# Kernel tuning notes

Hardware: AMD Instinct MI355X
Metric: run time of the kernel (lower is better)

The kernel has to match this reference:

```python
import jax, jax.numpy as jnp
import numpy as np

# Model dims (hardcoded by the hw-accurate numerics: >>6 mean -> d_model=64, 45/256 ~ 1/sqrt(32) -> head_dim=32)
D_MODEL = 64; N_HEADS = 2; HEAD_DIM = 32; D_FF = 256
N_LAYERS = 4; VOCAB = 8192; CTX = 1024; B = 4; T = 1024


def _ste(x, y):
    # forward value y, straight-through gradient of x
    return x + jax.lax.stop_gradient(y - x)


def ste_round_clamp(x, lo, hi):
    return _ste(x, jnp.clip(jnp.round(x), lo, hi))


def ste_round_clamp_int8(x):
    return ste_round_clamp(x, -128.0, 127.0)


def ste_shift_right(x, n):
    s = x * (0.5 ** n)
    return _ste(s, jnp.floor(s))


def ste_hw_int8(x):
    # hardware truncation to signed 8 bits (wrap-around, not clamp)
    return _ste(x, jnp.mod(x + 128.0, 256.0) - 128.0)


def bitlinear_hw(x, w):
    # ternary weights via STE (BitNet b1.58 style), int accumulate, >>6 requant, int8 clamp
    scale = jnp.maximum(jnp.mean(jnp.abs(w)), 1e-5)
    w_t = ste_round_clamp(w / scale, -1.0, 1.0)
    acc = jnp.einsum('btc,oc->bto', x, w_t)
    return ste_round_clamp_int8(ste_shift_right(acc, 6))


def rmsnorm_hw(x, weight):
    x_int = ste_round_clamp_int8(x)
    sum_sq = jnp.sum(x_int * x_int, axis=-1, keepdims=True)
    mean_sq = ste_shift_right(sum_sq, 6)                       # /64 == /d_model
    lut_idx = jnp.clip(ste_shift_right(mean_sq, 6), 0.0, 255.0)
    bin_center = jnp.maximum(lut_idx * 64.0 + 32.0, 1.0)
    inv_rms = ste_round_clamp(16384.0 / jnp.sqrt(bin_center), 0.0, 16383.0)
    w_c = weight + jax.lax.stop_gradient(jnp.clip(weight, -2.0, 2.0) - weight)
    gamma_q = ste_round_clamp(w_c * 1024.0, -32768.0, 32767.0)  # Q5.10
    p1 = ste_shift_right(x_int * inv_rms, 8)
    y = ste_shift_right(p1 * gamma_q, 10)
    return ste_round_clamp_int8(y)


def hw_softmax(scores):
    # 4-segment piecewise-linear exp + uint8 normalization (Softmax.scala)
    m = jnp.max(scores, axis=-1, keepdims=True)
    sh = scores - m
    ea = jnp.where(sh >= -3.0, 256.0 + sh * 64.0,
         jnp.where(sh >= -8.0, 64.0 + (sh + 3.0) * 11.0,
         jnp.where(sh >= -24.0, sh + 24.0, 0.0)))
    s = jnp.maximum(jnp.sum(ea, axis=-1, keepdims=True), 1.0)
    return ste_round_clamp(ea / s * 255.0, 0.0, 255.0)


def _forward(tokens, tok_emb, pos_emb, attn_norm_w, q_w, k_w, v_w, o_w,
             ff_norm_w, up_w, down_w, final_norm_w):
    positions = jnp.arange(T)
    tok_q = ste_round_clamp(tok_emb[tokens] * 1024.0, -32768.0, 32767.0)
    pos_q = ste_round_clamp(pos_emb[positions] * 1024.0, -32768.0, 32767.0)
    x = ste_hw_int8(ste_shift_right(tok_q + pos_q[None], 3))   # [B,T,D]
    causal = jnp.triu(jnp.ones((T, T), dtype=bool), k=1)
    for i in range(N_LAYERS):
        # attention block
        h = rmsnorm_hw(x, attn_norm_w[i])
        q = bitlinear_hw(h, q_w[i]).reshape(B, T, N_HEADS, HEAD_DIM).transpose(0, 2, 1, 3)
        k = bitlinear_hw(h, k_w[i]).reshape(B, T, N_HEADS, HEAD_DIM).transpose(0, 2, 1, 3)
        v = bitlinear_hw(h, v_w[i]).reshape(B, T, N_HEADS, HEAD_DIM).transpose(0, 2, 1, 3)
        scores = ste_shift_right(jnp.einsum('bhqd,bhkd->bhqk', q, k) * 45.0, 8)
        scores = jnp.where(causal, -32767.0, scores)
        probs = hw_softmax(scores)                              # uint8-valued
        a = ste_hw_int8(ste_shift_right(jnp.einsum('bhqk,bhkd->bhqd', probs, v), 8))
        a = a.transpose(0, 2, 1, 3).reshape(B, T, D_MODEL)
        a = bitlinear_hw(a, o_w[i])
        x = ste_hw_int8(x + a)
        # FFN block
        h = rmsnorm_hw(x, ff_norm_w[i])
        u = ste_round_clamp_int8(jax.nn.relu(bitlinear_hw(h, up_w[i])))
        x = ste_hw_int8(x + bitlinear_hw(u, down_w[i]))
    x = rmsnorm_hw(x, final_norm_w)
    # hw logits: INT8 activations x Q5.10 tied embedding, dequant + 1/sqrt(d) scale
    emb_q = ste_round_clamp(tok_emb * 1024.0, -32768.0, 32767.0)
    logits = jnp.einsum('btd,vd->btv', x, emb_q) * (D_MODEL ** -0.5 / 1024.0)
    return logits


def setup_inputs() -> dict:
    key = jax.random.key(0)
    ks = jax.random.split(key, 12)
    std = 0.02
    inp = {
        'tokens': jax.random.randint(ks[0], (B, T), 0, VOCAB),
        'tok_emb': jax.random.normal(ks[1], (VOCAB, D_MODEL), jnp.float32),  # default N(0,1)
        'pos_emb': std * jax.random.normal(ks[2], (CTX, D_MODEL), jnp.float32),
        'attn_norm_w': jnp.ones((N_LAYERS, D_MODEL), jnp.float32),
        'q_w': std * jax.random.normal(ks[3], (N_LAYERS, D_MODEL, D_MODEL), jnp.float32),
        'k_w': std * jax.random.normal(ks[4], (N_LAYERS, D_MODEL, D_MODEL), jnp.float32),
        'v_w': std * jax.random.normal(ks[5], (N_LAYERS, D_MODEL, D_MODEL), jnp.float32),
        'o_w': std * jax.random.normal(ks[6], (N_LAYERS, D_MODEL, D_MODEL), jnp.float32),
        'ff_norm_w': jnp.ones((N_LAYERS, D_MODEL), jnp.float32),
        'up_w': std * jax.random.normal(ks[7], (N_LAYERS, D_FF, D_MODEL), jnp.float32),
        'down_w': std * jax.random.normal(ks[8], (N_LAYERS, D_MODEL, D_FF), jnp.float32),
        'final_norm_w': jnp.ones((D_MODEL,), jnp.float32),
    }
    return inp


def reference(tokens, tok_emb, pos_emb, attn_norm_w, q_w, k_w, v_w, o_w,
              ff_norm_w, up_w, down_w, final_norm_w):
    return _forward(tokens, tok_emb, pos_emb, attn_norm_w, q_w, k_w, v_w, o_w,
                    ff_norm_w, up_w, down_w, final_norm_w)
```

## Files before the change

### kernel.cpp

```cpp
#include <hip/hip_runtime.h>
#include <stdint.h>

#define T_CTX 1024
#define DM 64
#define NH 2
#define HD 32
#define DFF 256
#define NVOCAB 8192

typedef int v4i __attribute__((ext_vector_type(4)));

__device__ __forceinline__ int clampi(int v, int lo, int hi){ return v<lo?lo:(v>hi?hi:v); }
__device__ __forceinline__ int wrap8(int v){ return ((v + 128) & 255) - 128; }
__device__ __forceinline__ int sdot4(int a, int b, int c){ return __builtin_amdgcn_sdot4(a, b, c, false); }

__device__ __forceinline__ int wave_reduce_add(int v){
  #pragma unroll
  for (int off = 1; off < 64; off <<= 1) v += __shfl_xor(v, off, 64);
  return v;
}
__device__ __forceinline__ int wave_reduce_max(int v){
  #pragma unroll
  for (int off = 1; off < 64; off <<= 1){ int o = __shfl_xor(v, off, 64); v = o > v ? o : v; }
  return v;
}

__device__ __forceinline__ int rmsnorm_one(int xv, int g){
  int ss  = wave_reduce_add(xv * xv);
  int ms  = ss >> 6;
  int lut = ms >> 6; if (lut > 255) lut = 255;
  int bc  = lut * 64 + 32;
  int inv = (int)__builtin_rint(16384.0 / __builtin_sqrt((double)bc));
  int p1  = (xv * inv) >> 8;
  int y   = (p1 * g) >> 10;
  return clampi(y, -128, 127);
}

__global__ __launch_bounds__(256) void prep_weights(
    const float* __restrict__ qw, const float* __restrict__ kw, const float* __restrict__ vw,
    const float* __restrict__ ow, const float* __restrict__ uw, const float* __restrict__ dw,
    const float* __restrict__ anw, const float* __restrict__ fnw, const float* __restrict__ finw,
    int8_t* __restrict__ wt, int16_t* __restrict__ gq)
{
  int tid = threadIdx.x;
  int bid = blockIdx.x;
  if (bid < 24) {
    int layer = bid / 6, kind = bid % 6;
    const float* src; int n; int off;
    switch (kind) {
      case 0:  src = qw + layer*4096;  n = 4096;  off = 0;     break;
      case 1:  src = kw + layer*4096;  n = 4096;  off = 4096;  break;
      case 2:  src = vw + layer*4096;  n = 4096;  off = 8192;  break;
      case 3:  src = ow + layer*4096;  n = 4096;  off = 12288; break;
      case 4:  src = uw + layer*16384; n = 16384; off = 16384; break;
      default: src = dw + layer*16384; n = 16384; off = 32768; break;
    }
    __shared__ double sred[256];
    double s = 0.0;
    for (int i = tid; i < n; i += 256) s += (double)__builtin_fabsf(src[i]);
    sred[tid] = s; __syncthreads();
    for (int st = 128; st > 0; st >>= 1){ if (tid < st) sred[tid] += sred[tid + st]; __syncthreads(); }
    float fs = (float)(sred[0] / (double)n);
    if (fs < 1e-5f) fs = 1e-5f;
    int8_t* dst = wt + layer*49152 + off;
    for (int i = tid; i < n; i += 256) {
      int t = (int)__builtin_rintf(src[i] / fs);
      dst[i] = (int8_t)clampi(t, -1, 1);
    }
  } else {
    for (int i = tid; i < 576; i += 256) {
      int norm = i >> 6, c = i & 63;
      const float* wsrc = (norm < 4) ? (anw + norm*64) : (norm < 8) ? (fnw + (norm-4)*64) : finw;
      float wv = wsrc[c];
      float wc = wv < -2.0f ? -2.0f : (wv > 2.0f ? 2.0f : wv);
      gq[i] = (int16_t)clampi((int)__builtin_rintf(wc * 1024.0f), -32768, 32767);
    }
  }
}

__global__ __launch_bounds__(256) void prep_emb_kernel(
    const float* __restrict__ tok_emb, int8_t* __restrict__ elo, int8_t* __restrict__ ehi)
{
  int i = blockIdx.x * 256 + threadIdx.x;
  if (i < NVOCAB * DM) {
    int e  = clampi((int)__builtin_rintf(tok_emb[i] * 1024.0f), -32768, 32767);
    int l  = ((e + 128) & 255) - 128;
    int hh = (e - l) >> 8;
    if (hh > 127) hh = 127;
    elo[i] = (int8_t)l; ehi[i] = (int8_t)hh;
  }
}

__global__ __launch_bounds__(256) void token_stage(
    const int* __restrict__ tokens, const float* __restrict__ tok_emb, const float* __restrict__ pos_emb,
    int8_t* __restrict__ x, const int8_t* __restrict__ aArr,
    int8_t* __restrict__ qA, int8_t* __restrict__ kA, int8_t* __restrict__ vT,
    const int8_t* __restrict__ wt, const int16_t* __restrict__ gq, int8_t* __restrict__ xf,
    int do_embed, int post_layer, int pre_layer, int do_final)
{
  __shared__ int8_t sh8[4][DFF];
  int w = threadIdx.x >> 6, lane = threadIdx.x & 63;
  int t = blockIdx.x * 4 + w;
  int8_t* myS = sh8[w];
  int xv;
  if (do_embed) {
    int tok = tokens[t];
    int s = t & (T_CTX - 1);
    int tq = clampi((int)__builtin_rintf(tok_emb[tok*DM + lane] * 1024.0f), -32768, 32767);
    int pq = clampi((int)__builtin_rintf(pos_emb[s*DM + lane] * 1024.0f), -32768, 32767);
    xv = wrap8((tq + pq) >> 3);
  } else {
    xv = (int)x[t*DM + lane];
  }
  if (post_layer >= 0) {
    const int8_t* wtL = wt + post_layer*49152;
    myS[lane] = aArr[t*DM + lane];
    __syncthreads();
    {
      const int* a4 = (const int*)myS;
      const int* wo = (const int*)(wtL + 12288);
      int acc = 0;
      #pragma unroll
      for (int i = 0; i < 16; i++) acc = sdot4(a4[i], wo[lane*16 + i], acc);
      xv = wrap8(xv + clampi(acc >> 6, -128, 127));
    }
    __syncthreads();
    int h2 = rmsnorm_one(xv, (int)gq[(4 + post_layer)*DM + lane]);
    myS[lane] = (int8_t)h2;
    __syncthreads();
    int uv[4];
    {
      const int* h4 = (const int*)myS;
      const int* wu = (const int*)(wtL + 16384);
      #pragma unroll
      for (int jj = 0; jj < 4; jj++) {
        int j = jj*64 + lane;
        int acc = 0;
        #pragma unroll
        for (int i = 0; i < 16; i++) acc = sdot4(h4[i], wu[j*16 + i], acc);
        int u = clampi(acc >> 6, -128, 127);
        uv[jj] = u < 0 ? 0 : u;
      }
    }
    __syncthreads();
    #pragma unroll
    for (int jj = 0; jj < 4; jj++) myS[jj*64 + lane] = (int8_t)uv[jj];
    __syncthreads();
    {
      const int* u4 = (const int*)myS;
      const int* wd = (const int*)(wtL + 32768);
      int acc = 0;
      #pragma unroll
      for (int i = 0; i < 64; i++) acc = sdot4(u4[i], wd[lane*64 + i], acc);
      xv = wrap8(xv + clampi(acc >> 6, -128, 127));
    }
    __syncthreads();
  }
  x[t*DM + lane] = (int8_t)xv;
  if (pre_layer >= 0) {
    int h = rmsnorm_one(xv, (int)gq[pre_layer*DM + lane]);
    myS[lane] = (int8_t)h;
    __syncthreads();
    const int8_t* wtL = wt + pre_layer*49152;
    const int* h4 = (const int*)myS;
    int b = t >> 10, s = t & (T_CTX - 1);
    int hh = lane >> 5, d = lane & 31;
    int bhh = b*NH + hh;
    {
      const int* wm = (const int*)(wtL + 0);
      int acc = 0;
      #pragma unroll
      for (int i = 0; i < 16; i++) acc = sdot4(h4[i], wm[lane*16 + i], acc);
      qA[(bhh*T_CTX + s)*HD + d] = (int8_t)clampi(acc >> 6, -128, 127);
    }
    {
      const int* wm = (const int*)(wtL + 4096);
      int acc = 0;
      #pragma unroll
      for (int i = 0; i < 16; i++) acc = sdot4(h4[i], wm[lane*16 + i], acc);
      kA[(bhh*T_CTX + s)*HD + d] = (int8_t)clampi(acc >> 6, -128, 127);
    }
    {
      const int* wm = (const int*)(wtL + 8192);
      int acc = 0;
      #pragma unroll
      for (int i = 0; i < 16; i++) acc = sdot4(h4[i], wm[lane*16 + i], acc);
      vT[(bhh*HD + d)*T_CTX + s] = (int8_t)clampi(acc >> 6, -128, 127);
    }
  }
  if (do_final) {
    int h = rmsnorm_one(xv, (int)gq[8*DM + lane]);
    xf[t*DM + lane] = (int8_t)h;
  }
}

__global__ __launch_bounds__(256) void attn_kernel(
    const int8_t* __restrict__ qA, const int8_t* __restrict__ kA, const int8_t* __restrict__ vT,
    int8_t* __restrict__ aOut)
{
  __shared__ int vt32[32*257];
  __shared__ int sp32[4][256];
  int w = threadIdx.x >> 6, lane = threadIdx.x & 63;
  int bh = blockIdx.x & 7, qblk = blockIdx.x >> 3;
  int qi = 1023 - 4*qblk - w;
  int b = bh >> 1, h = bh & 1;
  const int8_t* qBase = qA + bh*(T_CTX*HD);
  const int8_t* kBase = kA + bh*(T_CTX*HD);
  const int8_t* vTbh  = vT + bh*(HD*T_CTX);

  #pragma unroll
  for (int r = 0; r < 8; r++) {
    int d = r*4 + w;
    int4 v = *(const int4*)(vTbh + d*T_CTX + lane*16);
    int* dst = vt32 + d*257 + lane*4;
    dst[0] = v.x; dst[1] = v.y; dst[2] = v.z; dst[3] = v.w;
  }

  const int4* qr = (const int4*)(qBase + qi*HD);
  int4 qa = qr[0], qb = qr[1];
  int sc[16];
  int mloc = -(1 << 30);
  #pragma unroll
  for (int j = 0; j < 16; j++) {
    int k = lane + j*64;
    int s;
    if (k <= qi) {
      const int4* kr = (const int4*)(kBase + k*HD);
      int4 ka = kr[0], kb = kr[1];
      int d = 0;
      d = sdot4(qa.x, ka.x, d); d = sdot4(qa.y, ka.y, d);
      d = sdot4(qa.z, ka.z, d); d = sdot4(qa.w, ka.w, d);
      d = sdot4(qb.x, kb.x, d); d = sdot4(qb.y, kb.y, d);
      d = sdot4(qb.z, kb.z, d); d = sdot4(qb.w, kb.w, d);
      s = (d * 45) >> 8;
    } else s = -(1 << 30);
    sc[j] = s; if (s > mloc) mloc = s;
  }
  int m = wave_reduce_max(mloc);
  int ssum = 0;
  #pragma unroll
  for (int j = 0; j < 16; j++) {
    int k = lane + j*64;
    int e = 0;
    if (k <= qi) {
      int sh = sc[j] - m;
      e = (sh >= -3) ? (256 + sh*64)
        : (sh >= -8) ? (64 + (sh + 3)*11)
        : (sh >= -24) ? (sh + 24) : 0;
    }
    sc[j] = e; ssum += e;
  }
  int s0 = wave_reduce_add(ssum); if (s0 < 1) s0 = 1;
  float sf = (float)s0;
  uint8_t* spb = (uint8_t*)sp32[w];
  #pragma unroll
  for (int j = 0; j < 16; j++) {
    int k = lane + j*64;
    int p = (int)__builtin_rintf((float)sc[j] / sf * 255.0f);
    spb[k] = (uint8_t)clampi(p, 0, 255);
  }
  __syncthreads();

  int dg = lane & 7, kc = lane >> 3;
  const int* vr0 = vt32 + (dg*4 + 0)*257;
  const int* vr1 = vt32 + (dg*4 + 1)*257;
  const int* vr2 = vt32 + (dg*4 + 2)*257;
  const int* vr3 = vt32 + (dg*4 + 3)*257;
  const int* spw = sp32[w];
  int hi0=0, hi1=0, hi2=0, hi3=0, lo0=0, lo1=0, lo2=0, lo3=0;
  int cmax = qi >> 2;
  for (int c = kc; c <= cmax; c += 8) {
    int p4 = spw[c];
    int ph = (p4 >> 1) & 0x7f7f7f7f;
    int pl = p4 & 0x01010101;
    int v0 = vr0[c], v1 = vr1[c], v2 = vr2[c], v3 = vr3[c];
    hi0 = sdot4(ph, v0, hi0); lo0 = sdot4(pl, v0, lo0);
    hi1 = sdot4(ph, v1, hi1); lo1 = sdot4(pl, v1, lo1);
    hi2 = sdot4(ph, v2, hi2); lo2 = sdot4(pl, v2, lo2);
    hi3 = sdot4(ph, v3, hi3); lo3 = sdot4(pl, v3, lo3);
  }
  int a0 = 2*hi0 + lo0, a1 = 2*hi1 + lo1, a2 = 2*hi2 + lo2, a3 = 2*hi3 + lo3;
  #pragma unroll
  for (int off = 8; off < 64; off <<= 1) {
    a0 += __shfl_xor(a0, off, 64);
    a1 += __shfl_xor(a1, off, 64);
    a2 += __shfl_xor(a2, off, 64);
    a3 += __shfl_xor(a3, off, 64);
  }
  if (kc == 0) {
    int r0 = wrap8(a0 >> 8) & 255;
    int r1 = wrap8(a1 >> 8) & 255;
    int r2 = wrap8(a2 >> 8) & 255;
    int r3 = wrap8(a3 >> 8) & 255;
    int packed = r0 | (r1 << 8) | (r2 << 16) | (r3 << 24);
    *(int*)(aOut + (b*T_CTX + qi)*DM + h*HD + dg*4) = packed;
  }
}

__global__ __launch_bounds__(256) void logits_kernel(
    const int8_t* __restrict__ xf, const int8_t* __restrict__ elo, const int8_t* __restrict__ ehi,
    float* __restrict__ out)
{
  int w = threadIdx.x >> 6, lane = threadIdx.x & 63;
  int m = lane & 15, quad = lane >> 4;
  int tokBase = blockIdx.y * 64 + w * 16;
  v4i A = *(const v4i*)(xf + (tokBase + m)*DM + quad*16);
  #pragma unroll
  for (int tile = 0; tile < 8; tile++) {
    int vocBase = blockIdx.x * 128 + tile * 16;
    v4i Blo = *(const v4i*)(elo + (vocBase + m)*DM + quad*16);
    v4i Bhi = *(const v4i*)(ehi + (vocBase + m)*DM + quad*16);
    v4i zero = {0, 0, 0, 0};
    v4i dLo = __builtin_amdgcn_mfma_i32_16x16x64_i8(A, Blo, zero, 0, 0, 0);
    v4i dHi = __builtin_amdgcn_mfma_i32_16x16x64_i8(A, Bhi, zero, 0, 0, 0);
    #pragma unroll
    for (int r = 0; r < 4; r++) {
      int val = dLo[r] + (dHi[r] << 8);
      int row = tokBase + quad*4 + r;
      int col = vocBase + m;
      out[row*NVOCAB + col] = (float)val * 1.220703125e-4f;
    }
  }
}

extern "C" void kernel_launch(void* const* d_in, const int* in_sizes, int n_in,
                              void* d_out, int out_size, void* d_ws, size_t ws_size,
                              hipStream_t stream)
{
  const int*   tokens  = (const int*)d_in[0];
  const float* tok_emb = (const float*)d_in[1];
  const float* pos_emb = (const float*)d_in[2];
  const float* attn_nw = (const float*)d_in[3];
  const float* q_w     = (const float*)d_in[4];
  const float* k_w     = (const float*)d_in[5];
  const float* v_w     = (const float*)d_in[6];
  const float* o_w     = (const float*)d_in[7];
  const float* ff_nw   = (const float*)d_in[8];
  const float* up_w    = (const float*)d_in[9];
  const float* dn_w    = (const float*)d_in[10];
  const float* fin_nw  = (const float*)d_in[11];
  float* out = (float*)d_out;
  char* ws = (char*)d_ws;

  int8_t*  x   = (int8_t*)(ws + 0);
  int8_t*  a   = (int8_t*)(ws + 262144);
  int8_t*  qA  = (int8_t*)(ws + 524288);
  int8_t*  kA  = (int8_t*)(ws + 786432);
  int8_t*  vT  = (int8_t*)(ws + 1048576);
  int8_t*  wt  = (int8_t*)(ws + 1310720);
  int8_t*  elo = (int8_t*)(ws + 1507328);
  int8_t*  ehi = (int8_t*)(ws + 2031616);
  int16_t* gq  = (int16_t*)(ws + 2555904);
  int8_t*  xf  = (int8_t*)(ws + 2560000);

  prep_weights<<<25, 256, 0, stream>>>(q_w, k_w, v_w, o_w, up_w, dn_w, attn_nw, ff_nw, fin_nw, wt, gq);
  prep_emb_kernel<<<2048, 256, 0, stream>>>(tok_emb, elo, ehi);
  token_stage<<<1024, 256, 0, stream>>>(tokens, tok_emb, pos_emb, x, a, qA, kA, vT, wt, gq, xf,
                                        1, -1, 0, 0);
  for (int L = 0; L < 4; L++) {
    attn_kernel<<<2048, 256, 0, stream>>>(qA, kA, vT, a);
    int pre = (L < 3) ? (L + 1) : -1;
    int fin = (L == 3) ? 1 : 0;
    token_stage<<<1024, 256, 0, stream>>>(tokens, tok_emb, pos_emb, x, a, qA, kA, vT, wt, gq, xf,
                                          0, L, pre, fin);
  }
  logits_kernel<<<dim3(64, 64), 256, 0, stream>>>(xf, elo, ehi, out);
}
```

Baseline: 358.7 us.

## Fuse prep, embed, attention and token stages into one persistent kernel with grid barriers

Replaces eleven separate launches (weight prep, embedding prep, token stages, attention) with one persistent 512-block kernel that steps through the phases, separated by an atomic grid-wide barrier. Each block now handles 16 queries in attention, so the V tile staged in shared memory is reused across them, and each wave processes two tokens in the per-token stage. The aim is to remove launch gaps and cut redundant V loads. The cost is spin-wait barriers that assume all 512 blocks are co-resident, less parallelism per phase, and serialized query loops inside each block.

```diff
diff --git a/kernel.cpp b/kernel.cpp
--- a/kernel.cpp
+++ b/kernel.cpp
@@ -7,6 +7,7 @@
 #define HD 32
 #define DFF 256
 #define NVOCAB 8192
+#define NBLOCKS 512
 
 typedef int v4i __attribute__((ext_vector_type(4)));
 
@@ -23,6 +24,23 @@
   #pragma unroll
   for (int off = 1; off < 64; off <<= 1){ int o = __shfl_xor(v, off, 64); v = o > v ? o : v; }
   return v;
+}
+
+__device__ __forceinline__ void gbar(int* cnt, int* gen){
+  __syncthreads();
+  if (threadIdx.x == 0) {
+    int g = __hip_atomic_load(gen, __ATOMIC_RELAXED, __HIP_MEMORY_SCOPE_AGENT);
+    int prev = __hip_atomic_fetch_add(cnt, 1, __ATOMIC_ACQ_REL, __HIP_MEMORY_SCOPE_AGENT);
+    if (prev == NBLOCKS - 1) {
+      __hip_atomic_store(cnt, 0, __ATOMIC_RELAXED, __HIP_MEMORY_SCOPE_AGENT);
+      __hip_atomic_store(gen, g + 1, __ATOMIC_RELEASE, __HIP_MEMORY_SCOPE_AGENT);
+    } else {
+      while (__hip_atomic_load(gen, __ATOMIC_ACQUIRE, __HIP_MEMORY_SCOPE_AGENT) == g) {
+        __builtin_amdgcn_s_sleep(8);
+      }
+    }
+  }
+  __syncthreads();
 }
 
 __device__ __forceinline__ int rmsnorm_one(int xv, int g){
@@ -36,14 +54,213 @@
   return clampi(y, -128, 127);
 }
 
-__global__ __launch_bounds__(256) void prep_weights(
-    const float* __restrict__ qw, const float* __restrict__ kw, const float* __restrict__ vw,
-    const float* __restrict__ ow, const float* __restrict__ uw, const float* __restrict__ dw,
-    const float* __restrict__ anw, const float* __restrict__ fnw, const float* __restrict__ finw,
-    int8_t* __restrict__ wt, int16_t* __restrict__ gq)
-{
-  int tid = threadIdx.x;
-  int bid = blockIdx.x;
+__device__ __forceinline__ void do_qkv(int t, int xv, int L, int lane, int8_t* myS,
+    const int8_t* wt, const int16_t* gq, int8_t* qA, int8_t* kA, int8_t* vT)
+{
+  int h = rmsnorm_one(xv, (int)gq[L*DM + lane]);
+  myS[lane] = (int8_t)h;
+  __syncthreads();
+  const int8_t* wtL = wt + L*49152;
+  const int* h4 = (const int*)myS;
+  const int* wq = (const int*)(wtL + 0);
+  const int* wk = (const int*)(wtL + 4096);
+  const int* wv = (const int*)(wtL + 8192);
+  int b = t >> 10, s = t & (T_CTX - 1);
+  int hh = lane >> 5, d = lane & 31;
+  int bhh = b*NH + hh;
+  int accq = 0, acck = 0, accv = 0;
+  #pragma unroll
+  for (int i = 0; i < 16; i++) {
+    int hv = h4[i];
+    accq = sdot4(hv, wq[lane*16 + i], accq);
+    acck = sdot4(hv, wk[lane*16 + i], acck);
+    accv = sdot4(hv, wv[lane*16 + i], accv);
+  }
+  qA[(bhh*T_CTX + s)*HD + d] = (int8_t)clampi(accq >> 6, -128, 127);
+  kA[(bhh*T_CTX + s)*HD + d] = (int8_t)clampi(acck >> 6, -128, 127);
+  vT[(bhh*HD + d)*T_CTX + s] = (int8_t)clampi(accv >> 6, -128, 127);
+}
+
+__device__ __forceinline__ void attn_phase(int bid, int w, int lane,
+    const int8_t* __restrict__ qA, const int8_t* __restrict__ kA,
+    const int8_t* __restrict__ vT, int8_t* __restrict__ aOut, char* smemc)
+{
+  int bh = bid & 7, qgrp = bid >> 3;
+  int b = bh >> 1, h = bh & 1;
+  const int8_t* qBase = qA + bh*(T_CTX*HD);
+  const int8_t* kBase = kA + bh*(T_CTX*HD);
+  const int8_t* vTbh  = vT + bh*(HD*T_CTX);
+  int* vt32 = (int*)smemc;
+  #pragma unroll
+  for (int r = 0; r < 8; r++) {
+    int d = r*4 + w;
+    int4 v = *(const int4*)(vTbh + d*T_CTX + lane*16);
+    int* dst = vt32 + d*257 + lane*4;
+    dst[0] = v.x; dst[1] = v.y; dst[2] = v.z; dst[3] = v.w;
+  }
+  __syncthreads();
+  uint8_t* spb = (uint8_t*)(smemc + 32896 + w*1024);
+  const int* spw = (const int*)spb;
+  int dg = lane & 7, kc = lane >> 3;
+  const int* vr0 = vt32 + (dg*4 + 0)*257;
+  const int* vr1 = vt32 + (dg*4 + 1)*257;
+  const int* vr2 = vt32 + (dg*4 + 2)*257;
+  const int* vr3 = vt32 + (dg*4 + 3)*257;
+  #pragma unroll
+  for (int ri = 0; ri < 4; ri++) {
+    int i = w + ri*4;
+    int qi = i*64 + qgrp;
+    const int4* qr = (const int4*)(qBase + qi*HD);
+    int4 qa = qr[0], qb = qr[1];
+    int sc[16];
+    int mloc = -(1 << 30);
+    #pragma unroll
+    for (int j = 0; j < 16; j++) {
+      int k = lane + j*64;
+      int s;
+      if (k <= qi) {
+        const int4* kr = (const int4*)(kBase + k*HD);
+        int4 ka = kr[0], kb = kr[1];
+        int d0 = 0, d1 = 0;
+        d0 = sdot4(qa.x, ka.x, d0); d1 = sdot4(qa.y, ka.y, d1);
+        d0 = sdot4(qa.z, ka.z, d0); d1 = sdot4(qa.w, ka.w, d1);
+        d0 = sdot4(qb.x, kb.x, d0); d1 = sdot4(qb.y, kb.y, d1);
+        d0 = sdot4(qb.z, kb.z, d0); d1 = sdot4(qb.w, kb.w, d1);
+        s = ((d0 + d1) * 45) >> 8;
+      } else s = -(1 << 30);
+      sc[j] = s; if (s > mloc) mloc = s;
+    }
+    int m = wave_reduce_max(mloc);
+    int ssum = 0;
+    #pragma unroll
+    for (int j = 0; j < 16; j++) {
+      int k = lane + j*64;
+      int e = 0;
+      if (k <= qi) {
+        int sh = sc[j] - m;
+        e = (sh >= -3) ? (256 + sh*64)
+          : (sh >= -8) ? (64 + (sh + 3)*11)
+          : (sh >= -24) ? (sh + 24) : 0;
+      }
+      sc[j] = e; ssum += e;
+    }
+    int s0 = wave_reduce_add(ssum); if (s0 < 1) s0 = 1;
+    float sf = (float)s0;
+    #pragma unroll
+    for (int j = 0; j < 16; j++) {
+      int k = lane + j*64;
+      int p = (int)__builtin_rintf((float)sc[j] / sf * 255.0f);
+      spb[k] = (uint8_t)clampi(p, 0, 255);
+    }
+    __syncthreads();
+    int hi0=0, hi1=0, hi2=0, hi3=0, lo0=0, lo1=0, lo2=0, lo3=0;
+    int cmax = qi >> 2;
+    for (int c = kc; c <= cmax; c += 8) {
+      int p4 = spw[c];
+      int ph = (p4 >> 1) & 0x7f7f7f7f;
+      int pl = p4 & 0x01010101;
+      int v0 = vr0[c], v1 = vr1[c], v2 = vr2[c], v3 = vr3[c];
+      hi0 = sdot4(ph, v0, hi0); lo0 = sdot4(pl, v0, lo0);
+      hi1 = sdot4(ph, v1, hi1); lo1 = sdot4(pl, v1, lo1);
+      hi2 = sdot4(ph, v2, hi2); lo2 = sdot4(pl, v2, lo2);
+      hi3 = sdot4(ph, v3, hi3); lo3 = sdot4(pl, v3, lo3);
+    }
+    int a0 = 2*hi0 + lo0, a1 = 2*hi1 + lo1, a2 = 2*hi2 + lo2, a3 = 2*hi3 + lo3;
+    #pragma unroll
+    for (int off = 8; off < 64; off <<= 1) {
+      a0 += __shfl_xor(a0, off, 64);
+      a1 += __shfl_xor(a1, off, 64);
+      a2 += __shfl_xor(a2, off, 64);
+      a3 += __shfl_xor(a3, off, 64);
+    }
+    if (kc == 0) {
+      int r0 = wrap8(a0 >> 8) & 255;
+      int r1 = wrap8(a1 >> 8) & 255;
+      int r2 = wrap8(a2 >> 8) & 255;
+      int r3 = wrap8(a3 >> 8) & 255;
+      int packed = r0 | (r1 << 8) | (r2 << 16) | (r3 << 24);
+      *(int*)(aOut + (b*T_CTX + qi)*DM + h*HD + dg*4) = packed;
+    }
+    __syncthreads();
+  }
+}
+
+__device__ __forceinline__ void post_phase(int gw, int w, int lane, int L,
+    int8_t* x, const int8_t* __restrict__ aArr,
+    int8_t* qA, int8_t* kA, int8_t* vT,
+    const int8_t* __restrict__ wt, const int16_t* __restrict__ gq,
+    int8_t* xf, char* smemc)
+{
+  int8_t* myS = (int8_t*)smemc + w*DFF;
+  const int8_t* wtL = wt + L*49152;
+  for (int tt = 0; tt < 2; tt++) {
+    int t = gw*2 + tt;
+    int xv = (int)x[t*DM + lane];
+    myS[lane] = aArr[t*DM + lane];
+    __syncthreads();
+    {
+      const int* a4 = (const int*)myS;
+      const int* wo = (const int*)(wtL + 12288);
+      int acc = 0;
+      #pragma unroll
+      for (int i = 0; i < 16; i++) acc = sdot4(a4[i], wo[lane*16 + i], acc);
+      xv = wrap8(xv + clampi(acc >> 6, -128, 127));
+    }
+    __syncthreads();
+    int h2 = rmsnorm_one(xv, (int)gq[(4 + L)*DM + lane]);
+    myS[lane] = (int8_t)h2;
+    __syncthreads();
+    int uv[4];
+    {
+      const int* h4 = (const int*)myS;
+      const int* wu = (const int*)(wtL + 16384);
+      #pragma unroll
+      for (int jj = 0; jj < 4; jj++) {
+        int acc = 0;
+        #pragma unroll
+        for (int i = 0; i < 16; i++) acc = sdot4(h4[i], wu[(jj*64 + lane)*16 + i], acc);
+        int u = clampi(acc >> 6, -128, 127);
+        uv[jj] = u < 0 ? 0 : u;
+      }
+    }
+    __syncthreads();
+    #pragma unroll
+    for (int jj = 0; jj < 4; jj++) myS[jj*64 + lane] = (int8_t)uv[jj];
+    __syncthreads();
+    {
+      const int* u4 = (const int*)myS;
+      const int* wd = (const int*)(wtL + 32768);
+      int acc = 0;
+      #pragma unroll
+      for (int i = 0; i < 64; i++) acc = sdot4(u4[i], wd[lane*64 + i], acc);
+      xv = wrap8(xv + clampi(acc >> 6, -128, 127));
+    }
+    x[t*DM + lane] = (int8_t)xv;
+    __syncthreads();
+    if (L < 3) {
+      do_qkv(t, xv, L + 1, lane, myS, wt, gq, qA, kA, vT);
+    } else {
+      int h = rmsnorm_one(xv, (int)gq[8*DM + lane]);
+      xf[t*DM + lane] = (int8_t)h;
+    }
+    __syncthreads();
+  }
+}
+
+__global__ __launch_bounds__(256, 2) void mega(
+    const int* __restrict__ tokens, const float* __restrict__ tok_emb, const float* __restrict__ pos_emb,
+    const float* __restrict__ anw, const float* __restrict__ qw, const float* __restrict__ kw,
+    const float* __restrict__ vw, const float* __restrict__ ow, const float* __restrict__ fnw,
+    const float* __restrict__ uw, const float* __restrict__ dw, const float* __restrict__ finw,
+    int8_t* x, int8_t* a, int8_t* qA, int8_t* kA, int8_t* vT,
+    int8_t* wt, int16_t* gq, int8_t* elo, int8_t* ehi, int8_t* xf,
+    int* bar_cnt, int* bar_gen)
+{
+  __shared__ __align__(16) char smemc[36992];
+  int tid = threadIdx.x, bid = blockIdx.x;
+  int w = tid >> 6, lane = tid & 63;
+  int gw = bid*4 + w;
+
   if (bid < 24) {
     int layer = bid / 6, kind = bid % 6;
     const float* src; int n; int off;
@@ -55,7 +272,7 @@
       case 4:  src = uw + layer*16384; n = 16384; off = 16384; break;
       default: src = dw + layer*16384; n = 16384; off = 32768; break;
     }
-    __shared__ double sred[256];
+    double* sred = (double*)smemc;
     double s = 0.0;
     for (int i = tid; i < n; i += 256) s += (double)__builtin_fabsf(src[i]);
     sred[tid] = s; __syncthreads();
@@ -64,10 +281,10 @@
     if (fs < 1e-5f) fs = 1e-5f;
     int8_t* dst = wt + layer*49152 + off;
     for (int i = tid; i < n; i += 256) {
-      int t = (int)__builtin_rintf(src[i] / fs);
-      dst[i] = (int8_t)clampi(t, -1, 1);
-    }
-  } else {
+      int tq = (int)__builtin_rintf(src[i] / fs);
+      dst[i] = (int8_t)clampi(tq, -1, 1);
+    }
+  } else if (bid == 24) {
     for (int i = tid; i < 576; i += 256) {
       int norm = i >> 6, c = i & 63;
       const float* wsrc = (norm < 4) ? (anw + norm*64) : (norm < 8) ? (fnw + (norm-4)*64) : finw;
@@ -76,224 +293,39 @@
       gq[i] = (int16_t)clampi((int)__builtin_rintf(wc * 1024.0f), -32768, 32767);
     }
   }
-}
-
-__global__ __launch_bounds__(256) void prep_emb_kernel(
-    const float* __restrict__ tok_emb, int8_t* __restrict__ elo, int8_t* __restrict__ ehi)
-{
-  int i = blockIdx.x * 256 + threadIdx.x;
-  if (i < NVOCAB * DM) {
+  for (int i = bid*256 + tid; i < NVOCAB*DM; i += NBLOCKS*256) {
     int e  = clampi((int)__builtin_rintf(tok_emb[i] * 1024.0f), -32768, 32767);
     int l  = ((e + 128) & 255) - 128;
     int hh = (e - l) >> 8;
     if (hh > 127) hh = 127;
     elo[i] = (int8_t)l; ehi[i] = (int8_t)hh;
   }
-}
-
-__global__ __launch_bounds__(256) void token_stage(
-    const int* __restrict__ tokens, const float* __restrict__ tok_emb, const float* __restrict__ pos_emb,
-    int8_t* __restrict__ x, const int8_t* __restrict__ aArr,
-    int8_t* __restrict__ qA, int8_t* __restrict__ kA, int8_t* __restrict__ vT,
-    const int8_t* __restrict__ wt, const int16_t* __restrict__ gq, int8_t* __restrict__ xf,
-    int do_embed, int post_layer, int pre_layer, int do_final)
-{
-  __shared__ int8_t sh8[4][DFF];
-  int w = threadIdx.x >> 6, lane = threadIdx.x & 63;
-  int t = blockIdx.x * 4 + w;
-  int8_t* myS = sh8[w];
-  int xv;
-  if (do_embed) {
+  for (int i = bid*256 + tid; i < 4096*DM; i += NBLOCKS*256) {
+    int t = i >> 6, c = i & 63;
     int tok = tokens[t];
     int s = t & (T_CTX - 1);
-    int tq = clampi((int)__builtin_rintf(tok_emb[tok*DM + lane] * 1024.0f), -32768, 32767);
-    int pq = clampi((int)__builtin_rintf(pos_emb[s*DM + lane] * 1024.0f), -32768, 32767);
-    xv = wrap8((tq + pq) >> 3);
-  } else {
-    xv = (int)x[t*DM + lane];
-  }
-  if (post_layer >= 0) {
-    const int8_t* wtL = wt + post_layer*49152;
-    myS[lane] = aArr[t*DM + lane];
-    __syncthreads();
-    {
-      const int* a4 = (const int*)myS;
-      const int* wo = (const int*)(wtL + 12288);
-      int acc = 0;
-      #pragma unroll
-      for (int i = 0; i < 16; i++) acc = sdot4(a4[i], wo[lane*16 + i], acc);
-      xv = wrap8(xv + clampi(acc >> 6, -128, 127));
-    }
-    __syncthreads();
-    int h2 = rmsnorm_one(xv, (int)gq[(4 + post_layer)*DM + lane]);
-    myS[lane] = (int8_t)h2;
-    __syncthreads();
-    int uv[4];
-    {
-      const int* h4 = (const int*)myS;
-      const int* wu = (const int*)(wtL + 16384);
-      #pragma unroll
-      for (int jj = 0; jj < 4; jj++) {
-        int j = jj*64 + lane;
-        int acc = 0;
-        #pragma unroll
-        for (int i = 0; i < 16; i++) acc = sdot4(h4[i], wu[j*16 + i], acc);
-        int u = clampi(acc >> 6, -128, 127);
-        uv[jj] = u < 0 ? 0 : u;
-      }
-    }
-    __syncthreads();
-    #pragma unroll
-    for (int jj = 0; jj < 4; jj++) myS[jj*64 + lane] = (int8_t)uv[jj];
-    __syncthreads();
-    {
-      const int* u4 = (const int*)myS;
-      const int* wd = (const int*)(wtL + 32768);
-      int acc = 0;
-      #pragma unroll
-      for (int i = 0; i < 64; i++) acc = sdot4(u4[i], wd[lane*64 + i], acc);
-      xv = wrap8(xv + clampi(acc >> 6, -128, 127));
-    }
-    __syncthreads();
-  }
-  x[t*DM + lane] = (int8_t)xv;
-  if (pre_layer >= 0) {
-    int h = rmsnorm_one(xv, (int)gq[pre_layer*DM + lane]);
-    myS[lane] = (int8_t)h;
-    __syncthreads();
-    const int8_t* wtL = wt + pre_layer*49152;
-    const int* h4 = (const int*)myS;
-    int b = t >> 10, s = t & (T_CTX - 1);
-    int hh = lane >> 5, d = lane & 31;
-    int bhh = b*NH + hh;
-    {
-      const int* wm = (const int*)(wtL + 0);
-      int acc = 0;
-      #pragma unroll
-      for (int i = 0; i < 16; i++) acc = sdot4(h4[i], wm[lane*16 + i], acc);
-      qA[(bhh*T_CTX + s)*HD + d] = (int8_t)clampi(acc >> 6, -128, 127);
-    }
-    {
-      const int* wm = (const int*)(wtL + 4096);
-      int acc = 0;
-      #pragma unroll
-      for (int i = 0; i < 16; i++) acc = sdot4(h4[i], wm[lane*16 + i], acc);
-      kA[(bhh*T_CTX + s)*HD + d] = (int8_t)clampi(acc >> 6, -128, 127);
-    }
-    {
-      const int* wm = (const int*)(wtL + 8192);
-      int acc = 0;
-      #pragma unroll
-      for (int i = 0; i < 16; i++) acc = sdot4(h4[i], wm[lane*16 + i], acc);
-      vT[(bhh*HD + d)*T_CTX + s] = (int8_t)clampi(acc >> 6, -128, 127);
-    }
-  }
-  if (do_final) {
-    int h = rmsnorm_one(xv, (int)gq[8*DM + lane]);
-    xf[t*DM + lane] = (int8_t)h;
-  }
-}
-
-__global__ __launch_bounds__(256) void attn_kernel(
-    const int8_t* __restrict__ qA, const int8_t* __restrict__ kA, const int8_t* __restrict__ vT,
-    int8_t* __restrict__ aOut)
-{
-  __shared__ int vt32[32*257];
-  __shared__ int sp32[4][256];
-  int w = threadIdx.x >> 6, lane = threadIdx.x & 63;
-  int bh = blockIdx.x & 7, qblk = blockIdx.x >> 3;
-  int qi = 1023 - 4*qblk - w;
-  int b = bh >> 1, h = bh & 1;
-  const int8_t* qBase = qA + bh*(T_CTX*HD);
-  const int8_t* kBase = kA + bh*(T_CTX*HD);
-  const int8_t* vTbh  = vT + bh*(HD*T_CTX);
-
-  #pragma unroll
-  for (int r = 0; r < 8; r++) {
-    int d = r*4 + w;
-    int4 v = *(const int4*)(vTbh + d*T_CTX + lane*16);
-    int* dst = vt32 + d*257 + lane*4;
-    dst[0] = v.x; dst[1] = v.y; dst[2] = v.z; dst[3] = v.w;
-  }
-
-  const int4* qr = (const int4*)(qBase + qi*HD);
-  int4 qa = qr[0], qb = qr[1];
-  int sc[16];
-  int mloc = -(1 << 30);
-  #pragma unroll
-  for (int j = 0; j < 16; j++) {
-    int k = lane + j*64;
-    int s;
-    if (k <= qi) {
-      const int4* kr = (const int4*)(kBase + k*HD);
-      int4 ka = kr[0], kb = kr[1];
-      int d = 0;
-      d = sdot4(qa.x, ka.x, d); d = sdot4(qa.y, ka.y, d);
-      d = sdot4(qa.z, ka.z, d); d = sdot4(qa.w, ka.w, d);
-      d = sdot4(qb.x, kb.x, d); d = sdot4(qb.y, kb.y, d);
-      d = sdot4(qb.z, kb.z, d); d = sdot4(qb.w, kb.w, d);
-      s = (d * 45) >> 8;
-    } else s = -(1 << 30);
-    sc[j] = s; if (s > mloc) mloc = s;
-  }
-  int m = wave_reduce_max(mloc);
-  int ssum = 0;
-  #pragma unroll
-  for (int j = 0; j < 16; j++) {
-    int k = lane + j*64;
-    int e = 0;
-    if (k <= qi) {
-      int sh = sc[j] - m;
-      e = (sh >= -3) ? (256 + sh*64)
-        : (sh >= -8) ? (64 + (sh + 3)*11)
-        : (sh >= -24) ? (sh + 24) : 0;
-    }
-    sc[j] = e; ssum += e;
-  }
-  int s0 = wave_reduce_add(ssum); if (s0 < 1) s0 = 1;
-  float sf = (float)s0;
-  uint8_t* spb = (uint8_t*)sp32[w];
-  #pragma unroll
-  for (int j = 0; j < 16; j++) {
-    int k = lane + j*64;
-    int p = (int)__builtin_rintf((float)sc[j] / sf * 255.0f);
-    spb[k] = (uint8_t)clampi(p, 0, 255);
-  }
-  __syncthreads();
-
-  int dg = lane & 7, kc = lane >> 3;
-  const int* vr0 = vt32 + (dg*4 + 0)*257;
-  const int* vr1 = vt32 + (dg*4 + 1)*257;
-  const int* vr2 = vt32 + (dg*4 + 2)*257;
-  const int* vr3 = vt32 + (dg*4 + 3)*257;
-  const int* spw = sp32[w];
-  int hi0=0, hi1=0, hi2=0, hi3=0, lo0=0, lo1=0, lo2=0, lo3=0;
-  int cmax = qi >> 2;
-  for (int c = kc; c <= cmax; c += 8) {
-    int p4 = spw[c];
-    int ph = (p4 >> 1) & 0x7f7f7f7f;
-    int pl = p4 & 0x01010101;
-    int v0 = vr0[c], v1 = vr1[c], v2 = vr2[c], v3 = vr3[c];
-    hi0 = sdot4(ph, v0, hi0); lo0 = sdot4(pl, v0, lo0);
-    hi1 = sdot4(ph, v1, hi1); lo1 = sdot4(pl, v1, lo1);
-    hi2 = sdot4(ph, v2, hi2); lo2 = sdot4(pl, v2, lo2);
-    hi3 = sdot4(ph, v3, hi3); lo3 = sdot4(pl, v3, lo3);
-  }
-  int a0 = 2*hi0 + lo0, a1 = 2*hi1 + lo1, a2 = 2*hi2 + lo2, a3 = 2*hi3 + lo3;
-  #pragma unroll
-  for (int off = 8; off < 64; off <<= 1) {
-    a0 += __shfl_xor(a0, off, 64);
-    a1 += __shfl_xor(a1, off, 64);
-    a2 += __shfl_xor(a2, off, 64);
-    a3 += __shfl_xor(a3, off, 64);
-  }
-  if (kc == 0) {
-    int r0 = wrap8(a0 >> 8) & 255;
-    int r1 = wrap8(a1 >> 8) & 255;
-    int r2 = wrap8(a2 >> 8) & 255;
-    int r3 = wrap8(a3 >> 8) & 255;
-    int packed = r0 | (r1 << 8) | (r2 << 16) | (r3 << 24);
-    *(int*)(aOut + (b*T_CTX + qi)*DM + h*HD + dg*4) = packed;
+    int tq = clampi((int)__builtin_rintf(tok_emb[tok*DM + c] * 1024.0f), -32768, 32767);
+    int pq = clampi((int)__builtin_rintf(pos_emb[s*DM + c] * 1024.0f), -32768, 32767);
+    x[i] = (int8_t)wrap8((tq + pq) >> 3);
+  }
+  gbar(bar_cnt, bar_gen);
+
+  {
+    int8_t* myS = (int8_t*)smemc + w*DFF;
+    for (int tt = 0; tt < 2; tt++) {
+      int t = gw*2 + tt;
+      int xv = (int)x[t*DM + lane];
+      do_qkv(t, xv, 0, lane, myS, wt, gq, qA, kA, vT);
+      __syncthreads();
+    }
+  }
+  gbar(bar_cnt, bar_gen);
+
+  for (int L = 0; L < 4; L++) {
+    attn_phase(bid, w, lane, qA, kA, vT, a, smemc);
+    gbar(bar_cnt, bar_gen);
+    post_phase(gw, w, lane, L, x, a, qA, kA, vT, wt, gq, xf, smemc);
+    if (L < 3) gbar(bar_cnt, bar_gen);
   }
 }
 
@@ -352,17 +384,11 @@
   int8_t*  ehi = (int8_t*)(ws + 2031616);
   int16_t* gq  = (int16_t*)(ws + 2555904);
   int8_t*  xf  = (int8_t*)(ws + 2560000);
-
-  prep_weights<<<25, 256, 0, stream>>>(q_w, k_w, v_w, o_w, up_w, dn_w, attn_nw, ff_nw, fin_nw, wt, gq);
-  prep_emb_kernel<<<2048, 256, 0, stream>>>(tok_emb, elo, ehi);
-  token_stage<<<1024, 256, 0, stream>>>(tokens, tok_emb, pos_emb, x, a, qA, kA, vT, wt, gq, xf,
-                                        1, -1, 0, 0);
-  for (int L = 0; L < 4; L++) {
-    attn_kernel<<<2048, 256, 0, stream>>>(qA, kA, vT, a);
-    int pre = (L < 3) ? (L + 1) : -1;
-    int fin = (L == 3) ? 1 : 0;
-    token_stage<<<1024, 256, 0, stream>>>(tokens, tok_emb, pos_emb, x, a, qA, kA, vT, wt, gq, xf,
-                                          0, L, pre, fin);
-  }
+  int*     bar = (int*)(ws + 2822144);
+
+  hipMemsetAsync(bar, 0, 2*sizeof(int), stream);
+  mega<<<NBLOCKS, 256, 0, stream>>>(
+      tokens, tok_emb, pos_emb, attn_nw, q_w, k_w, v_w, o_w, ff_nw, up_w, dn_w, fin_nw,
+      x, a, qA, kA, vT, wt, gq, elo, ehi, xf, bar, bar + 1);
   logits_kernel<<<dim3(64, 64), 256, 0, stream>>>(xf, elo, ehi, out);
 }
```

Result: slower. 1.035 ms (+188.6%).
